# Optimization experiments

Hardware: AMD Instinct MI355X
Metric: run time of the kernel (lower is better)

## Reference

```python
import jax, jax.numpy as jnp
import numpy as np

N_NODES = 50000
N_EDGES = 800000
IN, HID, OUT = 128, 32, 64
HEADS = (4, 4, 4, 4)  # heads per layer (heads[0], heads[1], heads[1], heads[2])
NEG_SLOPE = 0.2


def gat_layer(h, src, dst, W, al, ar, b, activation):
    """One DGL-style GATConv. h: [N, Din]; W: [Din, H*F]; al, ar: [H, F]; b: [H*F]."""
    n = h.shape[0]
    H, F = al.shape
    feat = (h @ W).reshape(n, H, F)                       # [N, H, F]
    el = jnp.sum(feat * al, axis=-1)                      # [N, H]
    er = jnp.sum(feat * ar, axis=-1)                      # [N, H]
    e = jax.nn.leaky_relu(el[src] + er[dst], NEG_SLOPE)   # [E, H]
    # segment softmax over incoming edges of each dst node
    m = jax.ops.segment_max(e, dst, num_segments=n)       # [N, H]
    ex = jnp.exp(e - m[dst])                              # [E, H]
    denom = jax.ops.segment_sum(ex, dst, num_segments=n)  # [N, H]
    alpha = ex / jnp.maximum(denom[dst], 1e-9)            # [E, H]
    msg = feat[src] * alpha[:, :, None]                   # [E, H, F]
    out = jax.ops.segment_sum(msg, dst, num_segments=n) + b.reshape(H, F)
    return activation(out) if activation is not None else out


def setup_inputs() -> dict:
    key = jax.random.key(0)
    ks = jax.random.split(key, 20)
    x = jax.random.normal(ks[0], (N_NODES, IN), dtype=jnp.float32)
    src = jax.random.randint(ks[1], (N_EDGES,), 0, N_NODES, dtype=jnp.int32)
    dst = jax.random.randint(ks[2], (N_EDGES,), 0, N_NODES, dtype=jnp.int32)
    dims = [(IN, HEADS[0], HID), (HID * HEADS[0], HEADS[1], HID),
            (HID * HEADS[1], HEADS[2], HID), (HID * HEADS[2], HEADS[3], OUT)]
    inp = {"x": x, "src": src, "dst": dst}
    k = 3
    for i, (din, h, f) in enumerate(dims, start=1):
        inp[f"W{i}"] = jax.random.normal(ks[k], (din, h * f), dtype=jnp.float32) * 0.05; k += 1
        inp[f"al{i}"] = jax.random.normal(ks[k], (h, f), dtype=jnp.float32) * 0.05; k += 1
        inp[f"ar{i}"] = jax.random.normal(ks[k], (h, f), dtype=jnp.float32) * 0.05; k += 1
        inp[f"b{i}"] = jnp.zeros((h * f,), dtype=jnp.float32)
    return inp


def reference(x, src, dst, W1, al1, ar1, b1, W2, al2, ar2, b2,
              W3, al3, ar3, b3, W4, al4, ar4, b4):
    elu = jax.nn.elu
    h = gat_layer(x, src, dst, W1, al1, ar1, b1, elu).reshape(N_NODES, -1)   # flatten heads
    h = gat_layer(h, src, dst, W2, al2, ar2, b2, elu).reshape(N_NODES, -1)
    h = gat_layer(h, src, dst, W3, al3, ar3, b3, elu).reshape(N_NODES, -1)
    h = gat_layer(h, src, dst, W4, al4, ar4, b4, None).mean(axis=1)          # mean over heads
    return h
```

## Files before the change

### kernel.cpp

```cpp
#include <hip/hip_runtime.h>
#include <hip/hip_fp16.h>

#define N_NODES 50000
#define N_EDGES 800000

typedef _Float16 h8 __attribute__((ext_vector_type(8)));
typedef float f4 __attribute__((ext_vector_type(4)));

__device__ __forceinline__ float lrelu(float x){ return x > 0.f ? x : 0.2f*x; }
__device__ __forceinline__ float eluf (float x){ return x > 0.f ? x : __expf(x)-1.f; }

__global__ void k_histwt(const int* __restrict__ dst, int* __restrict__ cnt,
                         const float* __restrict__ W1, const float* __restrict__ W2,
                         const float* __restrict__ W3, const float* __restrict__ W4,
                         _Float16* __restrict__ wt){
  int b = blockIdx.x;
  if (b < 3125){
    int e = b*256 + threadIdx.x;
    if (e < N_EDGES) atomicAdd(&cnt[dst[e]], 1);
  } else {
    int id = (b - 3125)*256 + threadIdx.x;
    if (id < 81920){
      const float* W; int HF; int loc;
      if (id < 16384)      { W = W1; HF = 128; loc = id; }
      else if (id < 32768) { W = W2; HF = 128; loc = id - 16384; }
      else if (id < 49152) { W = W3; HF = 128; loc = id - 32768; }
      else                 { W = W4; HF = 256; loc = id - 49152; }
      int n = loc >> 7, k = loc & 127;
      wt[id] = (_Float16)W[(size_t)k*HF + n];
    }
  }
}

__global__ void k_scan1(const int* __restrict__ cnt, int* __restrict__ offs, int* __restrict__ bsum){
  __shared__ int tmp[256];
  int tid = threadIdx.x; int i = blockIdx.x*256 + tid;
  int v = (i < N_NODES) ? cnt[i] : 0;
  tmp[tid] = v; __syncthreads();
  for (int d = 1; d < 256; d <<= 1){
    int t = (tid >= d) ? tmp[tid-d] : 0;
    __syncthreads();
    tmp[tid] += t;
    __syncthreads();
  }
  if (i < N_NODES) offs[i] = tmp[tid] - v;
  if (tid == 255) bsum[blockIdx.x] = tmp[tid];
}

__global__ void k_scan2(int* __restrict__ bsum, int nb){
  __shared__ int tmp[256];
  int tid = threadIdx.x;
  int v = (tid < nb) ? bsum[tid] : 0;
  tmp[tid] = v; __syncthreads();
  for (int d = 1; d < 256; d <<= 1){
    int t = (tid >= d) ? tmp[tid-d] : 0;
    __syncthreads();
    tmp[tid] += t;
    __syncthreads();
  }
  if (tid < nb) bsum[tid] = tmp[tid] - v;
}

__global__ void k_scan3(int* __restrict__ offs, const int* __restrict__ bsum, int* __restrict__ cur){
  int i = blockIdx.x*256 + threadIdx.x;
  if (i < N_NODES){
    int o = offs[i] + bsum[blockIdx.x];
    offs[i] = o; cur[i] = o;
  }
  if (i == 0) offs[N_NODES] = N_EDGES;
}

__global__ void k_scatter(const int* __restrict__ src, const int* __restrict__ dst,
                          int* __restrict__ cur, int* __restrict__ csr_src){
  int e = blockIdx.x*256 + threadIdx.x;
  if (e < N_EDGES){
    int pos = atomicAdd(&cur[dst[e]], 1);
    csr_src[pos] = src[e];
  }
}

template<int HF, bool AHALF>
__global__ __launch_bounds__(256) void k_gemm(const void* __restrict__ Ain,
        const _Float16* __restrict__ Wt,
        __half* __restrict__ feat,
        const float* __restrict__ al, const float* __restrict__ ar,
        float* __restrict__ el, float* __restrict__ er){
  __shared__ char lds[49152];
  char* Alds = lds;
  char* Blds = lds + 32768;
  _Float16* Clds = (_Float16*)lds;
  const int tid  = threadIdx.x;
  const int row0 = blockIdx.x * 128;
  const int col0 = blockIdx.y * 64;

  if (AHALF){
    const __half* A16 = (const __half*)Ain;
    #pragma unroll
    for (int i = 0; i < 8; ++i){
      int flat = i*256 + tid;
      int r = flat >> 4, ch = flat & 15;
      uint4 v = make_uint4(0,0,0,0);
      if (row0 + r < N_NODES) v = *(const uint4*)&A16[(size_t)(row0+r)*128 + ch*8];
      *(uint4*)(Alds + ((r*256 + ch*16) ^ ((r&7)<<4))) = v;
    }
  } else {
    const float* A32 = (const float*)Ain;
    #pragma unroll
    for (int i = 0; i < 8; ++i){
      int flat = i*256 + tid;
      int r = flat >> 4, ch = flat & 15;
      h8 hv = {};
      if (row0 + r < N_NODES){
        float4 f0 = *(const float4*)&A32[(size_t)(row0+r)*128 + ch*8];
        float4 f1 = *(const float4*)&A32[(size_t)(row0+r)*128 + ch*8 + 4];
        hv[0]=(_Float16)f0.x; hv[1]=(_Float16)f0.y; hv[2]=(_Float16)f0.z; hv[3]=(_Float16)f0.w;
        hv[4]=(_Float16)f1.x; hv[5]=(_Float16)f1.y; hv[6]=(_Float16)f1.z; hv[7]=(_Float16)f1.w;
      }
      *(h8*)(Alds + ((r*256 + ch*16) ^ ((r&7)<<4))) = hv;
    }
  }
  #pragma unroll
  for (int i = 0; i < 4; ++i){
    int flat = i*256 + tid;
    int n = flat >> 4, ch = flat & 15;
    uint4 v = *(const uint4*)&Wt[(size_t)(col0+n)*128 + ch*8];
    *(uint4*)(Blds + ((n*256 + ch*16) ^ ((n&7)<<4))) = v;
  }
  __syncthreads();

  const int l = tid & 63, w = tid >> 6;
  f4 acc[2][4] = {};
  const int rA0  = w*32 + (l & 15);
  const int rA1  = rA0 + 16;
  const int nB   = (l & 15);
  const int ksel = (l >> 4) * 16;
  #pragma unroll
  for (int kb = 0; kb < 4; ++kb){
    int kofs = kb*64 + ksel;
    h8 a0 = *(const h8*)(Alds + ((rA0*256 + kofs) ^ ((rA0&7)<<4)));
    h8 a1 = *(const h8*)(Alds + ((rA1*256 + kofs) ^ ((rA1&7)<<4)));
    h8 b[4];
    #pragma unroll
    for (int nf = 0; nf < 4; ++nf){
      int n = nB + nf*16;
      b[nf] = *(const h8*)(Blds + ((n*256 + kofs) ^ ((n&7)<<4)));
    }
    #pragma unroll
    for (int nf = 0; nf < 4; ++nf){
      acc[0][nf] = __builtin_amdgcn_mfma_f32_16x16x32_f16(a0, b[nf], acc[0][nf], 0, 0, 0);
      acc[1][nf] = __builtin_amdgcn_mfma_f32_16x16x32_f16(a1, b[nf], acc[1][nf], 0, 0, 0);
    }
  }
  __syncthreads();

  #pragma unroll
  for (int mf = 0; mf < 2; ++mf){
    int rloc = w*32 + mf*16 + (l>>4)*4;
    #pragma unroll
    for (int nf = 0; nf < 4; ++nf){
      int c = nf*16 + (l&15);
      #pragma unroll
      for (int reg = 0; reg < 4; ++reg)
        Clds[(rloc+reg)*80 + c] = (_Float16)acc[mf][nf][reg];
    }
  }
  __syncthreads();

  constexpr int F = HF/4;
  int ch = l & 7;
  float4 al0 = *(const float4*)&al[col0 + ch*8];
  float4 al1 = *(const float4*)&al[col0 + ch*8 + 4];
  float4 ar0 = *(const float4*)&ar[col0 + ch*8];
  float4 ar1 = *(const float4*)&ar[col0 + ch*8 + 4];
  #pragma unroll
  for (int i = 0; i < 4; ++i){
    int rloc = i*32 + w*8 + (l>>3);
    int grow = row0 + rloc;
    h8 hv = *(const h8*)&Clds[rloc*80 + ch*8];
    if (grow < N_NODES)
      *(uint4*)&feat[(size_t)grow*HF + col0 + ch*8] = *(uint4*)&hv;
    float f0=(float)hv[0], f1=(float)hv[1], f2=(float)hv[2], f3=(float)hv[3];
    float f4_=(float)hv[4], f5=(float)hv[5], f6=(float)hv[6], f7=(float)hv[7];
    float pl = f0*al0.x + f1*al0.y + f2*al0.z + f3*al0.w
             + f4_*al1.x + f5*al1.y + f6*al1.z + f7*al1.w;
    float pr = f0*ar0.x + f1*ar0.y + f2*ar0.z + f3*ar0.w
             + f4_*ar1.x + f5*ar1.y + f6*ar1.z + f7*ar1.w;
    pl += __shfl_xor(pl, 1); pl += __shfl_xor(pl, 2);
    pr += __shfl_xor(pr, 1); pr += __shfl_xor(pr, 2);
    if (F == 64){ pl += __shfl_xor(pl, 4); pr += __shfl_xor(pr, 4); }
    bool lead = (F == 32) ? ((l & 3) == 0) : ((l & 7) == 0);
    if (lead && grow < N_NODES){
      int h = (col0 + ch*8) / F;
      el[grow*4 + h] = pl;
      er[grow*4 + h] = pr;
    }
  }
}

template<int F, bool FINAL, int LAYER>
__global__ __launch_bounds__(256) void k_agg(const int* __restrict__ offs,
        const int* __restrict__ csr_src, const float* __restrict__ el,
        const float* __restrict__ er, const __half* __restrict__ feat,
        const float* __restrict__ bias, void* __restrict__ out){
  int tid  = threadIdx.x;
  int wv   = tid >> 6;
  int lane = tid & 63;
  int n = blockIdx.x*4 + wv;
  int beg = offs[n], end = offs[n+1];
  float4 er4 = ((const float4*)er)[n];
  int ej = lane & 15, hj = lane >> 4;
  float er_hj = (hj==0) ? er4.x : (hj==1) ? er4.y : (hj==2) ? er4.z : er4.w;

  if (F == 32){
    int quarter = lane >> 4;
    int l4      = lane & 15;
    int h       = l4 >> 2;
    float a0=0.f,a1=0.f,a2=0.f,a3=0.f,a4=0.f,a5=0.f,a6=0.f,a7=0.f,ds=0.f;
    for (int cbeg = beg; cbeg < end; cbeg += 32){
      int m = end - cbeg; if (m > 32) m = 32;
      int sa = 0, sb = 0; float eva = 0.f, evb = 0.f;
      if (ej < m)      { sa = csr_src[cbeg + ej];      eva = __expf(lrelu(el[sa*4 + hj] + er_hj)); }
      if (16 + ej < m) { sb = csr_src[cbeg + 16 + ej]; evb = __expf(lrelu(el[sb*4 + hj] + er_hj)); }
      #pragma unroll 4
      for (int i = 0; i < 32; i += 4){
        int e = i + quarter;
        int s; float ev;
        if (i < 16){ s = __shfl(sa, e & 15); ev = __shfl(eva, (h<<4)|(e & 15)); }
        else       { s = __shfl(sb, e & 15); ev = __shfl(evb, (h<<4)|(e & 15)); }
        if (e < m){
          ds += ev;
          uint4 raw = *(const uint4*)&feat[(size_t)s*128 + l4*8];
          const __half2* hp = reinterpret_cast<const __half2*>(&raw);
          float2 f0 = __half22float2(hp[0]);
          float2 f1 = __half22float2(hp[1]);
          float2 f2 = __half22float2(hp[2]);
          float2 f3 = __half22float2(hp[3]);
          a0 += ev*f0.x; a1 += ev*f0.y; a2 += ev*f1.x; a3 += ev*f1.y;
          a4 += ev*f2.x; a5 += ev*f2.y; a6 += ev*f3.x; a7 += ev*f3.y;
        }
      }
    }
    ds += __shfl_xor(ds, 16); ds += __shfl_xor(ds, 32);
    a0 += __shfl_xor(a0, 16); a0 += __shfl_xor(a0, 32);
    a1 += __shfl_xor(a1, 16); a1 += __shfl_xor(a1, 32);
    a2 += __shfl_xor(a2, 16); a2 += __shfl_xor(a2, 32);
    a3 += __shfl_xor(a3, 16); a3 += __shfl_xor(a3, 32);
    a4 += __shfl_xor(a4, 16); a4 += __shfl_xor(a4, 32);
    a5 += __shfl_xor(a5, 16); a5 += __shfl_xor(a5, 32);
    a6 += __shfl_xor(a6, 16); a6 += __shfl_xor(a6, 32);
    a7 += __shfl_xor(a7, 16); a7 += __shfl_xor(a7, 32);
    if (quarter == 0){
      float rden = 1.f / fmaxf(ds, 1e-9f);
      float4 b0 = *(const float4*)&bias[l4*8];
      float4 b1 = *(const float4*)&bias[l4*8 + 4];
      float o0 = eluf(a0*rden + b0.x);
      float o1 = eluf(a1*rden + b0.y);
      float o2 = eluf(a2*rden + b0.z);
      float o3 = eluf(a3*rden + b0.w);
      float o4 = eluf(a4*rden + b1.x);
      float o5 = eluf(a5*rden + b1.y);
      float o6 = eluf(a6*rden + b1.z);
      float o7 = eluf(a7*rden + b1.w);
      __half* outh = (__half*)out;
      h8 hv;
      hv[0]=(_Float16)o0; hv[1]=(_Float16)o1; hv[2]=(_Float16)o2; hv[3]=(_Float16)o3;
      hv[4]=(_Float16)o4; hv[5]=(_Float16)o5; hv[6]=(_Float16)o6; hv[7]=(_Float16)o7;
      *(uint4*)&outh[(size_t)n*128 + l4*8] = *(uint4*)&hv;
    }
  } else {
    int hw  = lane >> 5;
    int l5  = lane & 31;
    int h   = l5 >> 3;
    float a0=0.f,a1=0.f,a2=0.f,a3=0.f,a4=0.f,a5=0.f,a6=0.f,a7=0.f,ds=0.f;
    for (int cbeg = beg; cbeg < end; cbeg += 32){
      int m = end - cbeg; if (m > 32) m = 32;
      int sa = 0, sb = 0; float eva = 0.f, evb = 0.f;
      if (ej < m)      { sa = csr_src[cbeg + ej];      eva = __expf(lrelu(el[sa*4 + hj] + er_hj)); }
      if (16 + ej < m) { sb = csr_src[cbeg + 16 + ej]; evb = __expf(lrelu(el[sb*4 + hj] + er_hj)); }
      #pragma unroll 4
      for (int i = 0; i < 32; i += 2){
        int e = i + hw;
        int s; float ev;
        if (i < 16){ s = __shfl(sa, e & 15); ev = __shfl(eva, (h<<4)|(e & 15)); }
        else       { s = __shfl(sb, e & 15); ev = __shfl(evb, (h<<4)|(e & 15)); }
        if (e < m){
          ds += ev;
          uint4 raw = *(const uint4*)&feat[(size_t)s*256 + l5*8];
          const __half2* hp = reinterpret_cast<const __half2*>(&raw);
          float2 f0 = __half22float2(hp[0]);
          float2 f1 = __half22float2(hp[1]);
          float2 f2 = __half22float2(hp[2]);
          float2 f3 = __half22float2(hp[3]);
          a0 += ev*f0.x; a1 += ev*f0.y; a2 += ev*f1.x; a3 += ev*f1.y;
          a4 += ev*f2.x; a5 += ev*f2.y; a6 += ev*f3.x; a7 += ev*f3.y;
        }
      }
    }
    ds += __shfl_xor(ds, 32);
    a0 += __shfl_xor(a0, 32); a1 += __shfl_xor(a1, 32);
    a2 += __shfl_xor(a2, 32); a3 += __shfl_xor(a3, 32);
    a4 += __shfl_xor(a4, 32); a5 += __shfl_xor(a5, 32);
    a6 += __shfl_xor(a6, 32); a7 += __shfl_xor(a7, 32);
    float rden = 1.f / fmaxf(ds, 1e-9f);
    float4 b0 = *(const float4*)&bias[l5*8];
    float4 b1 = *(const float4*)&bias[l5*8 + 4];
    float v0 = a0*rden + b0.x;
    float v1 = a1*rden + b0.y;
    float v2 = a2*rden + b0.z;
    float v3 = a3*rden + b0.w;
    float v4 = a4*rden + b1.x;
    float v5 = a5*rden + b1.y;
    float v6 = a6*rden + b1.z;
    float v7 = a7*rden + b1.w;
    v0 += __shfl_xor(v0, 8); v0 += __shfl_xor(v0, 16);
    v1 += __shfl_xor(v1, 8); v1 += __shfl_xor(v1, 16);
    v2 += __shfl_xor(v2, 8); v2 += __shfl_xor(v2, 16);
    v3 += __shfl_xor(v3, 8); v3 += __shfl_xor(v3, 16);
    v4 += __shfl_xor(v4, 8); v4 += __shfl_xor(v4, 16);
    v5 += __shfl_xor(v5, 8); v5 += __shfl_xor(v5, 16);
    v6 += __shfl_xor(v6, 8); v6 += __shfl_xor(v6, 16);
    v7 += __shfl_xor(v7, 8); v7 += __shfl_xor(v7, 16);
    if (hw == 0 && l5 < 8){
      float* outf = (float*)out;
      *(float4*)&outf[(size_t)n*64 + l5*8] =
        make_float4(v0*0.25f, v1*0.25f, v2*0.25f, v3*0.25f);
      *(float4*)&outf[(size_t)n*64 + l5*8 + 4] =
        make_float4(v4*0.25f, v5*0.25f, v6*0.25f, v7*0.25f);
    }
  }
}

extern "C" void kernel_launch(void* const* d_in, const int* in_sizes, int n_in,
                              void* d_out, int out_size, void* d_ws, size_t ws_size,
                              hipStream_t stream){
  const float* x   = (const float*)d_in[0];
  const int*   src = (const int*)  d_in[1];
  const int*   dst = (const int*)  d_in[2];
  const float* W[4]  = {(const float*)d_in[3],  (const float*)d_in[7],
                        (const float*)d_in[11], (const float*)d_in[15]};
  const float* al[4] = {(const float*)d_in[4],  (const float*)d_in[8],
                        (const float*)d_in[12], (const float*)d_in[16]};
  const float* ar[4] = {(const float*)d_in[5],  (const float*)d_in[9],
                        (const float*)d_in[13], (const float*)d_in[17]};
  const float* b[4]  = {(const float*)d_in[6],  (const float*)d_in[10],
                        (const float*)d_in[14], (const float*)d_in[18]};

  char* ws = (char*)d_ws;
  __half*    bufH = (__half*)   (ws);
  __half*    feat = (__half*)   (ws + 25600000);
  _Float16*  wt   = (_Float16*) (ws + 51200000);
  float*     el   = (float*)    (ws + 76800000);
  float*     er   = (float*)    (ws + 77600000);
  int*       offs = (int*)      (ws + 78400000);
  int*       cur  = (int*)      (ws + 78600032);
  int*       bsum = (int*)      (ws + 78800032);
  int*   csr_src  = (int*)      (ws + 78801056);

  (void)hipMemsetAsync(cur, 0, N_NODES*sizeof(int), stream);
  k_histwt <<<3445, 256, 0, stream>>>(dst, cur, W[0], W[1], W[2], W[3], wt);
  k_scan1  <<<196,  256, 0, stream>>>(cur, offs, bsum);
  k_scan2  <<<1,    256, 0, stream>>>(bsum, 196);
  k_scan3  <<<196,  256, 0, stream>>>(offs, bsum, cur);
  k_scatter<<<3125, 256, 0, stream>>>(src, dst, cur, csr_src);

  k_gemm<128,false><<<dim3(391,2), 256, 0, stream>>>(x, wt, feat, al[0], ar[0], el, er);
  k_agg<32,false,1><<<12500, 256, 0, stream>>>(offs, csr_src, el, er, feat, b[0], bufH);

  k_gemm<128,true><<<dim3(391,2), 256, 0, stream>>>(bufH, wt + 16384, feat, al[1], ar[1], el, er);
  k_agg<32,false,2><<<12500, 256, 0, stream>>>(offs, csr_src, el, er, feat, b[1], bufH);

  k_gemm<128,true><<<dim3(391,2), 256, 0, stream>>>(bufH, wt + 32768, feat, al[2], ar[2], el, er);
  k_agg<32,false,3><<<12500, 256, 0, stream>>>(offs, csr_src, el, er, feat, b[2], bufH);

  k_gemm<256,true><<<dim3(391,4), 256, 0, stream>>>(bufH, wt + 49152, feat, al[3], ar[3], el, er);
  k_agg<64,true,4><<<12500, 256, 0, stream>>>(offs, csr_src, el, er, feat, b[3], d_out);
}
```

Baseline: 443.7 us.

## Precompute per-edge attention exponentials in separate kernel and stage via LDS

Adds a csr_dst array and a per-layer k_edge kernel that computes exp(leaky_relu(el[src]+er[dst])) for all four heads per CSR edge and stores them. The aggregation kernel then stages 64 edges' source ids and weights in shared memory instead of gathering el and recomputing exp per head with shuffles. This is meant to remove scattered el gathers and shuffle overhead from the aggregation loop. In exchange it adds an extra launch per layer plus a 12.8MB write and read of edge weights. The LDS sync relies only on a waitcnt with no barrier, which is valid only because each wavefront uses its own slice.

```diff
diff --git a/kernel.cpp b/kernel.cpp
--- a/kernel.cpp
+++ b/kernel.cpp
@@ -71,12 +71,31 @@
 }
 
 __global__ void k_scatter(const int* __restrict__ src, const int* __restrict__ dst,
-                          int* __restrict__ cur, int* __restrict__ csr_src){
+                          int* __restrict__ cur, int* __restrict__ csr_src,
+                          int* __restrict__ csr_dst){
   int e = blockIdx.x*256 + threadIdx.x;
   if (e < N_EDGES){
-    int pos = atomicAdd(&cur[dst[e]], 1);
+    int d = dst[e];
+    int pos = atomicAdd(&cur[d], 1);
     csr_src[pos] = src[e];
-  }
+    csr_dst[pos] = d;
+  }
+}
+
+__global__ __launch_bounds__(256) void k_edge(const int* __restrict__ csr_src,
+        const int* __restrict__ csr_dst, const float* __restrict__ el,
+        const float* __restrict__ er, float* __restrict__ ev){
+  int e = blockIdx.x*256 + threadIdx.x;
+  if (e >= N_EDGES) return;
+  int s = csr_src[e], d = csr_dst[e];
+  float4 e4 = ((const float4*)el)[s];
+  float4 r4 = ((const float4*)er)[d];
+  float4 v;
+  v.x = __expf(lrelu(e4.x + r4.x));
+  v.y = __expf(lrelu(e4.y + r4.y));
+  v.z = __expf(lrelu(e4.z + r4.z));
+  v.w = __expf(lrelu(e4.w + r4.w));
+  ((float4*)ev)[e] = v;
 }
 
 template<int HF, bool AHALF>
@@ -199,46 +218,47 @@
 
 template<int F, bool FINAL, int LAYER>
 __global__ __launch_bounds__(256) void k_agg(const int* __restrict__ offs,
-        const int* __restrict__ csr_src, const float* __restrict__ el,
-        const float* __restrict__ er, const __half* __restrict__ feat,
+        const int* __restrict__ csr_src, const float* __restrict__ ev,
+        const __half* __restrict__ feat,
         const float* __restrict__ bias, void* __restrict__ out){
+  __shared__ float s_ev[4][64][4];
+  __shared__ int   s_src[4][64];
   int tid  = threadIdx.x;
   int wv   = tid >> 6;
   int lane = tid & 63;
   int n = blockIdx.x*4 + wv;
   int beg = offs[n], end = offs[n+1];
-  float4 er4 = ((const float4*)er)[n];
-  int ej = lane & 15, hj = lane >> 4;
-  float er_hj = (hj==0) ? er4.x : (hj==1) ? er4.y : (hj==2) ? er4.z : er4.w;
 
   if (F == 32){
     int quarter = lane >> 4;
     int l4      = lane & 15;
     int h       = l4 >> 2;
     float a0=0.f,a1=0.f,a2=0.f,a3=0.f,a4=0.f,a5=0.f,a6=0.f,a7=0.f,ds=0.f;
-    for (int cbeg = beg; cbeg < end; cbeg += 32){
-      int m = end - cbeg; if (m > 32) m = 32;
-      int sa = 0, sb = 0; float eva = 0.f, evb = 0.f;
-      if (ej < m)      { sa = csr_src[cbeg + ej];      eva = __expf(lrelu(el[sa*4 + hj] + er_hj)); }
-      if (16 + ej < m) { sb = csr_src[cbeg + 16 + ej]; evb = __expf(lrelu(el[sb*4 + hj] + er_hj)); }
+    for (int cbeg = beg; cbeg < end; cbeg += 64){
+      int m = end - cbeg; if (m > 64) m = 64;
+      if (lane < m){
+        s_src[wv][lane] = csr_src[cbeg + lane];
+        *(float4*)&s_ev[wv][lane][0] = *(const float4*)&ev[(size_t)(cbeg + lane)*4];
+      }
+      asm volatile("s_waitcnt lgkmcnt(0)" ::: "memory");
       #pragma unroll 4
-      for (int i = 0; i < 32; i += 4){
+      for (int i = 0; i < m; i += 4){
         int e = i + quarter;
-        int s; float ev;
-        if (i < 16){ s = __shfl(sa, e & 15); ev = __shfl(eva, (h<<4)|(e & 15)); }
-        else       { s = __shfl(sb, e & 15); ev = __shfl(evb, (h<<4)|(e & 15)); }
         if (e < m){
-          ds += ev;
+          int s = s_src[wv][e];
+          float w = s_ev[wv][e][h];
+          ds += w;
           uint4 raw = *(const uint4*)&feat[(size_t)s*128 + l4*8];
           const __half2* hp = reinterpret_cast<const __half2*>(&raw);
           float2 f0 = __half22float2(hp[0]);
           float2 f1 = __half22float2(hp[1]);
           float2 f2 = __half22float2(hp[2]);
           float2 f3 = __half22float2(hp[3]);
-          a0 += ev*f0.x; a1 += ev*f0.y; a2 += ev*f1.x; a3 += ev*f1.y;
-          a4 += ev*f2.x; a5 += ev*f2.y; a6 += ev*f3.x; a7 += ev*f3.y;
+          a0 += w*f0.x; a1 += w*f0.y; a2 += w*f1.x; a3 += w*f1.y;
+          a4 += w*f2.x; a5 += w*f2.y; a6 += w*f3.x; a7 += w*f3.y;
         }
       }
+      asm volatile("" ::: "memory");
     }
     ds += __shfl_xor(ds, 16); ds += __shfl_xor(ds, 32);
     a0 += __shfl_xor(a0, 16); a0 += __shfl_xor(a0, 32);
@@ -272,29 +292,31 @@
     int l5  = lane & 31;
     int h   = l5 >> 3;
     float a0=0.f,a1=0.f,a2=0.f,a3=0.f,a4=0.f,a5=0.f,a6=0.f,a7=0.f,ds=0.f;
-    for (int cbeg = beg; cbeg < end; cbeg += 32){
-      int m = end - cbeg; if (m > 32) m = 32;
-      int sa = 0, sb = 0; float eva = 0.f, evb = 0.f;
-      if (ej < m)      { sa = csr_src[cbeg + ej];      eva = __expf(lrelu(el[sa*4 + hj] + er_hj)); }
-      if (16 + ej < m) { sb = csr_src[cbeg + 16 + ej]; evb = __expf(lrelu(el[sb*4 + hj] + er_hj)); }
+    for (int cbeg = beg; cbeg < end; cbeg += 64){
+      int m = end - cbeg; if (m > 64) m = 64;
+      if (lane < m){
+        s_src[wv][lane] = csr_src[cbeg + lane];
+        *(float4*)&s_ev[wv][lane][0] = *(const float4*)&ev[(size_t)(cbeg + lane)*4];
+      }
+      asm volatile("s_waitcnt lgkmcnt(0)" ::: "memory");
       #pragma unroll 4
-      for (int i = 0; i < 32; i += 2){
+      for (int i = 0; i < m; i += 2){
         int e = i + hw;
-        int s; float ev;
-        if (i < 16){ s = __shfl(sa, e & 15); ev = __shfl(eva, (h<<4)|(e & 15)); }
-        else       { s = __shfl(sb, e & 15); ev = __shfl(evb, (h<<4)|(e & 15)); }
         if (e < m){
-          ds += ev;
+          int s = s_src[wv][e];
+          float w = s_ev[wv][e][h];
+          ds += w;
           uint4 raw = *(const uint4*)&feat[(size_t)s*256 + l5*8];
           const __half2* hp = reinterpret_cast<const __half2*>(&raw);
           float2 f0 = __half22float2(hp[0]);
           float2 f1 = __half22float2(hp[1]);
           float2 f2 = __half22float2(hp[2]);
           float2 f3 = __half22float2(hp[3]);
-          a0 += ev*f0.x; a1 += ev*f0.y; a2 += ev*f1.x; a3 += ev*f1.y;
-          a4 += ev*f2.x; a5 += ev*f2.y; a6 += ev*f3.x; a7 += ev*f3.y;
+          a0 += w*f0.x; a1 += w*f0.y; a2 += w*f1.x; a3 += w*f1.y;
+          a4 += w*f2.x; a5 += w*f2.y; a6 += w*f3.x; a7 += w*f3.y;
         }
       }
+      asm volatile("" ::: "memory");
     }
     ds += __shfl_xor(ds, 32);
     a0 += __shfl_xor(a0, 32); a1 += __shfl_xor(a1, 32);
@@ -346,32 +368,38 @@
                         (const float*)d_in[14], (const float*)d_in[18]};
 
   char* ws = (char*)d_ws;
-  __half*    bufH = (__half*)   (ws);
-  __half*    feat = (__half*)   (ws + 25600000);
-  _Float16*  wt   = (_Float16*) (ws + 51200000);
-  float*     el   = (float*)    (ws + 76800000);
-  float*     er   = (float*)    (ws + 77600000);
-  int*       offs = (int*)      (ws + 78400000);
-  int*       cur  = (int*)      (ws + 78600032);
-  int*       bsum = (int*)      (ws + 78800032);
-  int*   csr_src  = (int*)      (ws + 78801056);
+  __half*    bufH    = (__half*)   (ws);
+  __half*    feat    = (__half*)   (ws + 25600000);
+  _Float16*  wt      = (_Float16*) (ws + 51200000);
+  int*       csr_dst = (int*)      (ws + 51400000);
+  float*     ev      = (float*)    (ws + 60000000);
+  float*     el      = (float*)    (ws + 76800000);
+  float*     er      = (float*)    (ws + 77600000);
+  int*       offs    = (int*)      (ws + 78400000);
+  int*       cur     = (int*)      (ws + 78600032);
+  int*       bsum    = (int*)      (ws + 78800032);
+  int*       csr_src = (int*)      (ws + 78801056);
 
   (void)hipMemsetAsync(cur, 0, N_NODES*sizeof(int), stream);
   k_histwt <<<3445, 256, 0, stream>>>(dst, cur, W[0], W[1], W[2], W[3], wt);
   k_scan1  <<<196,  256, 0, stream>>>(cur, offs, bsum);
   k_scan2  <<<1,    256, 0, stream>>>(bsum, 196);
   k_scan3  <<<196,  256, 0, stream>>>(offs, bsum, cur);
-  k_scatter<<<3125, 256, 0, stream>>>(src, dst, cur, csr_src);
+  k_scatter<<<3125, 256, 0, stream>>>(src, dst, cur, csr_src, csr_dst);
 
   k_gemm<128,false><<<dim3(391,2), 256, 0, stream>>>(x, wt, feat, al[0], ar[0], el, er);
-  k_agg<32,false,1><<<12500, 256, 0, stream>>>(offs, csr_src, el, er, feat, b[0], bufH);
+  k_edge<<<3125, 256, 0, stream>>>(csr_src, csr_dst, el, er, ev);
+  k_agg<32,false,1><<<12500, 256, 0, stream>>>(offs, csr_src, ev, feat, b[0], bufH);
 
   k_gemm<128,true><<<dim3(391,2), 256, 0, stream>>>(bufH, wt + 16384, feat, al[1], ar[1], el, er);
-  k_agg<32,false,2><<<12500, 256, 0, stream>>>(offs, csr_src, el, er, feat, b[1], bufH);
+  k_edge<<<3125, 256, 0, stream>>>(csr_src, csr_dst, el, er, ev);
+  k_agg<32,false,2><<<12500, 256, 0, stream>>>(offs, csr_src, ev, feat, b[1], bufH);
 
   k_gemm<128,true><<<dim3(391,2), 256, 0, stream>>>(bufH, wt + 32768, feat, al[2], ar[2], el, er);
-  k_agg<32,false,3><<<12500, 256, 0, stream>>>(offs, csr_src, el, er, feat, b[2], bufH);
+  k_edge<<<3125, 256, 0, stream>>>(csr_src, csr_dst, el, er, ev);
+  k_agg<32,false,3><<<12500, 256, 0, stream>>>(offs, csr_src, ev, feat, b[2], bufH);
 
   k_gemm<256,true><<<dim3(391,4), 256, 0, stream>>>(bufH, wt + 49152, feat, al[3], ar[3], el, er);
-  k_agg<64,true,4><<<12500, 256, 0, stream>>>(offs, csr_src, el, er, feat, b[3], d_out);
-}
+  k_edge<<<3125, 256, 0, stream>>>(csr_src, csr_dst, el, er, ev);
+  k_agg<64,true,4><<<12500, 256, 0, stream>>>(offs, csr_src, ev, feat, b[3], d_out);
+}
```

New measurement: 451.5 us. Within noise of the previous version (+1.8%).
